# Kernel optimization log

Hardware: AMD Instinct MI355X
Metric: run time of the kernel (lower is better)

Reference implementation:

```python
import jax, jax.numpy as jnp
import numpy as np

HUGE = 1e8  # stand-in for ops.HUGE_INT

B, P, Q, PD, QD = 16, 1024, 512, 768, 768


def setup_inputs() -> dict:
    key = jax.random.key(0)
    k1, k2, k3, k4, k5 = jax.random.split(key, 5)
    p = jax.random.normal(k1, (B, P, PD), dtype=jnp.float32)
    q = jax.random.normal(k2, (B, Q, QD), dtype=jnp.float32)
    # True = padded position (masked out before softmax)
    p_masks = jax.random.randint(k3, (B, P), 0, 2).astype(bool)
    q_masks = jax.random.randint(k4, (B, Q), 0, 2).astype(bool)
    # projection weight of Linear(q_dim, p_dim, bias=False): [p_dim, q_dim]
    W = jax.random.normal(k5, (PD, QD), dtype=jnp.float32) / np.sqrt(QD)
    return {"p": p, "q": q, "p_masks": p_masks, "q_masks": q_masks, "W": W}


def reference(p, q, p_masks, q_masks, W):
    # q_proj = project(q): [B,Q,p_dim]; dropout=0.0 -> identity
    q_proj = jnp.einsum('bqd,pd->bqp', q, W)
    # affinity = p @ q_proj^T : [B,P,Q]
    affinity = jnp.einsum('bpd,bqd->bpq', p, q_proj)
    # normalize over dim 1 with padding mask broadcast over last dim
    attn_over_p = jax.nn.softmax(
        jnp.where(p_masks[:, :, None], -HUGE, affinity), axis=1)  # [B,P,Q]
    attn_over_q = jax.nn.softmax(
        jnp.where(q_masks[:, :, None], -HUGE, jnp.swapaxes(affinity, 1, 2)), axis=1)  # [B,Q,P]
    # attn(weights[B,W2,W3], cand[B,W2,C3]) -> [B,W3,C3] = weights^T @ cand
    q_to_p_attn_vec = jnp.einsum('bpq,bpd->bqd', attn_over_p, p)  # [B,Q,p_dim]
    cand = jnp.concatenate([q, q_to_p_attn_vec], axis=2)  # [B,Q,q_dim+p_dim]
    p_to_q_attn_vec = jnp.einsum('bqp,bqc->bpc', attn_over_q, cand)  # [B,P,q_dim+p_dim]
    return (p_to_q_attn_vec, q_to_p_attn_vec)
```

## Files before the change

### kernel.cpp

```cpp
#include <hip/hip_runtime.h>
#include <math.h>

constexpr int B_  = 16;
constexpr int P_  = 1024;
constexpr int Q_  = 512;
constexpr int PD_ = 768;
constexpr int QD_ = 768;
constexpr int CD_ = 1536;

#define HUGE_NEG (-1e8f)

typedef __attribute__((ext_vector_type(8))) _Float16 f16x8;
typedef __attribute__((ext_vector_type(4))) _Float16 f16x4;
typedef __attribute__((ext_vector_type(4))) float f32x4;

__device__ __forceinline__ void dma16(const void* g, void* l) {
  __builtin_amdgcn_global_load_lds((__attribute__((address_space(1))) void*)g,
                                   (__attribute__((address_space(3))) void*)l,
                                   16, 0, 0);
}

__global__ __launch_bounds__(256) void k_cvt(const float* __restrict__ src,
                                             _Float16* __restrict__ dst, int n8) {
  int i = blockIdx.x * 256 + threadIdx.x;
  if (i >= n8) return;
  float4 a = ((const float4*)src)[2 * i];
  float4 b = ((const float4*)src)[2 * i + 1];
  f16x8 o = {(_Float16)a.x, (_Float16)a.y, (_Float16)a.z, (_Float16)a.w,
             (_Float16)b.x, (_Float16)b.y, (_Float16)b.z, (_Float16)b.w};
  ((f16x8*)dst)[i] = o;
}

__global__ __launch_bounds__(256) void k_prep(const float* __restrict__ src,
                                              _Float16* __restrict__ dst16,
                                              _Float16* __restrict__ dstT,
                                              int R, int C, size_t tBatch) {
  __shared__ _Float16 T[64][72];
  int r0 = blockIdx.x * 64, c0 = blockIdx.y * 64, b = blockIdx.z;
  const float* S = src + (size_t)b * R * C;
  _Float16* D16 = dst16 + (size_t)b * R * C;
  int tid = threadIdx.x;
  int rr = tid >> 4;
  int cc = (tid & 15) * 4;
#pragma unroll
  for (int k = 0; k < 4; ++k) {
    int r = rr + k * 16;
    float4 v = *(const float4*)(S + (size_t)(r0 + r) * C + c0 + cc);
    f16x4 h = {(_Float16)v.x, (_Float16)v.y, (_Float16)v.z, (_Float16)v.w};
    *(f16x4*)(D16 + (size_t)(r0 + r) * C + c0 + cc) = h;
    T[cc + 0][r] = h[0];
    T[cc + 1][r] = h[1];
    T[cc + 2][r] = h[2];
    T[cc + 3][r] = h[3];
  }
  __syncthreads();
  int cr = tid >> 2;
  int rc = (tid & 3) * 16;
  _Float16* D = dstT + (size_t)b * tBatch + (size_t)(c0 + cr) * R + r0;
  *(f16x8*)(D + rc) = *(f16x8*)&T[cr][rc];
  *(f16x8*)(D + rc + 8) = *(f16x8*)&T[cr][rc + 8];
}

__global__ __launch_bounds__(256) void k_rowmerge(
    const float* __restrict__ rpm, const float* __restrict__ rps,
    float* __restrict__ rowmax, float* __restrict__ rowsum) {
  int idx = blockIdx.x * 256 + threadIdx.x;
  int b = idx >> 10, p = idx & 1023;
  float m = -INFINITY;
#pragma unroll
  for (int z = 0; z < 4; ++z) m = fmaxf(m, rpm[(b * 4 + z) * P_ + p]);
  float s = 0.f;
#pragma unroll
  for (int z = 0; z < 4; ++z)
    s += rps[(b * 4 + z) * P_ + p] * __expf(rpm[(b * 4 + z) * P_ + p] - m);
  rowmax[idx] = m;
  rowsum[idx] = s;
}

__global__ __launch_bounds__(256) void k_colmerge(
    const float* __restrict__ pmax_part, const float* __restrict__ psum_part,
    float* __restrict__ colmax, float* __restrict__ colsum) {
  int b = blockIdx.x;
  int q = blockIdx.y * 256 + threadIdx.x;
  float m = -INFINITY;
#pragma unroll
  for (int z = 0; z < 8; ++z) m = fmaxf(m, pmax_part[(b * 8 + z) * Q_ + q]);
  float s = 0.f;
#pragma unroll
  for (int z = 0; z < 8; ++z)
    s += psum_part[(b * 8 + z) * Q_ + q] *
         __expf(pmax_part[(b * 8 + z) * Q_ + q] - m);
  colmax[b * Q_ + q] = m;
  colsum[b * Q_ + q] = s;
}

__global__ __launch_bounds__(256) void k_w(
    const float* __restrict__ aff, const int* __restrict__ pmask,
    const int* __restrict__ qmask, const float* __restrict__ rowmax,
    const float* __restrict__ rowsum, const float* __restrict__ colmax,
    const float* __restrict__ colsum, _Float16* __restrict__ WP,
    _Float16* __restrict__ WQ) {
  __shared__ _Float16 T[64][72];
  __shared__ float rmx[64], rin[64], cmx[64], cin[64];
  int p0 = blockIdx.x * 64, q0 = blockIdx.y * 64, b = blockIdx.z;
  int tid = threadIdx.x;
  if (tid < 64) {
    rmx[tid] = rowmax[b * P_ + p0 + tid];
    rin[tid] = 1.0f / rowsum[b * P_ + p0 + tid];
  } else if (tid < 128) {
    int t = tid - 64;
    cmx[t] = colmax[b * Q_ + q0 + t];
    cin[t] = 1.0f / colsum[b * Q_ + q0 + t];
  }
  __syncthreads();
  const float* A = aff + (size_t)b * P_ * Q_;
  const int* pm = pmask + b * P_;
  int rr = tid >> 4;
  int cc = (tid & 15) * 4;
  int4 qm4 = *(const int4*)(qmask + b * Q_ + q0 + cc);
  int qm[4] = {qm4.x, qm4.y, qm4.z, qm4.w};
#pragma unroll
  for (int k = 0; k < 4; ++k) {
    int r = rr + k * 16;
    int msk = pm[p0 + r];
    float4 v = *(const float4*)(A + (size_t)(p0 + r) * Q_ + q0 + cc);
    float vv[4] = {v.x, v.y, v.z, v.w};
    f16x4 wp;
#pragma unroll
    for (int j = 0; j < 4; ++j) {
      wp[j] = (_Float16)(__expf((qm[j] ? HUGE_NEG : vv[j]) - rmx[r]) * rin[r]);
      T[cc + j][r] =
          (_Float16)(__expf((msk ? HUGE_NEG : vv[j]) - cmx[cc + j]) * cin[cc + j]);
    }
    *(f16x4*)(WP + ((size_t)b * P_ + p0 + r) * Q_ + q0 + cc) = wp;
  }
  __syncthreads();
  int cr = tid >> 2;
  int rc = (tid & 3) * 16;
  _Float16* D = WQ + ((size_t)b * Q_ + q0 + cr) * P_ + p0;
  *(f16x8*)(D + rc) = *(f16x8*)&T[cr][rc];
  *(f16x8*)(D + rc + 8) = *(f16x8*)&T[cr][rc + 8];
}

template <int NT, int LDA, int LDB>
__device__ __forceinline__ void gemm_core(const _Float16* __restrict__ Ab,
                                          const _Float16* __restrict__ Bb,
                                          _Float16* As, _Float16* Bs,
                                          f32x4 (&acc)[4][4], int w, int l) {
  constexpr int TSZ = 128 * 32;
  int rA = w * 32 + (l >> 2);
  int sA = ((l & 3) ^ ((rA >> 1) & 3)) * 8;
  int fr = l & 15;
  int fsw = (((l >> 4) ^ ((fr >> 1) & 3))) * 8;
  int wr = w >> 1, wc = w & 1;

  auto stage = [&](int buf, int t) {
    const _Float16* ga = Ab + (size_t)rA * LDA + t * 32 + sA;
    const _Float16* gb = Bb + (size_t)rA * LDB + t * 32 + sA;
    _Float16* la = As + buf * TSZ + (w * 32) * 32;
    _Float16* lb = Bs + buf * TSZ + (w * 32) * 32;
    dma16(ga, la);
    dma16(ga + 16 * LDA, la + 16 * 32);
    dma16(gb, lb);
    dma16(gb + 16 * LDB, lb + 16 * 32);
  };
  auto compute = [&](int buf) {
    const _Float16* A0 = As + buf * TSZ;
    const _Float16* B0 = Bs + buf * TSZ;
    f16x8 a[4];
#pragma unroll
    for (int m = 0; m < 4; ++m)
      a[m] = *(const f16x8*)(A0 + (wr * 64 + m * 16 + fr) * 32 + fsw);
#pragma unroll
    for (int n = 0; n < 4; ++n) {
      f16x8 bn = *(const f16x8*)(B0 + (wc * 64 + n * 16 + fr) * 32 + fsw);
#pragma unroll
      for (int m = 0; m < 4; ++m)
        acc[m][n] =
            __builtin_amdgcn_mfma_f32_16x16x32_f16(a[m], bn, acc[m][n], 0, 0, 0);
    }
  };

  stage(0, 0);
  stage(1, 1);
  int b0 = 0, b1 = 1, b2 = 2;
#pragma unroll 3
  for (int t = 0; t < NT - 2; ++t) {
    stage(b2, t + 2);
    asm volatile("s_waitcnt vmcnt(8)" ::: "memory");
    __builtin_amdgcn_s_barrier();
    __builtin_amdgcn_sched_barrier(0);
    compute(b0);
    __builtin_amdgcn_s_barrier();
    int tmp = b0; b0 = b1; b1 = b2; b2 = tmp;
  }
  asm volatile("s_waitcnt vmcnt(4)" ::: "memory");
  __builtin_amdgcn_s_barrier();
  __builtin_amdgcn_sched_barrier(0);
  compute(b0);
  __builtin_amdgcn_s_barrier();
  asm volatile("s_waitcnt vmcnt(0)" ::: "memory");
  __builtin_amdgcn_s_barrier();
  __builtin_amdgcn_sched_barrier(0);
  compute(b1);
}

#define SWZ_DECODE(GX, GY)                                          \
  int lin = blockIdx.x + (GX) * (blockIdx.y + (GY) * blockIdx.z);   \
  constexpr int NWG = (GX) * (GY) * B_;                             \
  int w8 = (lin & 7) * (NWG / 8) + (lin >> 3);                      \
  int j0 = (w8 % (GX)) * 128;                                       \
  int t_ = w8 / (GX);                                               \
  int i0 = (t_ % (GY)) * 128;                                       \
  int b = t_ / (GY);

__global__ __launch_bounds__(256) void k1_proj(const _Float16* __restrict__ q16,
                                               const _Float16* __restrict__ W16,
                                               _Float16* __restrict__ qp) {
  __shared__ alignas(16) _Float16 As[3 * 128 * 32];
  __shared__ alignas(16) _Float16 Bs[3 * 128 * 32];
  SWZ_DECODE(PD_ / 128, Q_ / 128)
  int tid = threadIdx.x, w = tid >> 6, l = tid & 63;
  f32x4 acc[4][4];
#pragma unroll
  for (int m = 0; m < 4; ++m)
#pragma unroll
    for (int n = 0; n < 4; ++n) acc[m][n] = (f32x4){0.f, 0.f, 0.f, 0.f};
  gemm_core<QD_ / 32, QD_, QD_>(q16 + (size_t)b * Q_ * QD_ + (size_t)i0 * QD_,
                                W16 + (size_t)j0 * QD_, As, Bs, acc, w, l);
  int wr = w >> 1, wc = w & 1, fr = l & 15, fq = l >> 4;
  _Float16* O = qp + (size_t)b * Q_ * PD_;
#pragma unroll
  for (int m = 0; m < 4; ++m) {
    int rl = wr * 64 + m * 16 + fq * 4;
#pragma unroll
    for (int n = 0; n < 4; ++n) {
      int cl = wc * 64 + n * 16 + fr;
#pragma unroll
      for (int r = 0; r < 4; ++r)
        O[(size_t)(i0 + rl + r) * PD_ + j0 + cl] = (_Float16)acc[m][n][r];
    }
  }
}

__global__ __launch_bounds__(256) void k2_aff(
    const _Float16* __restrict__ p16, const _Float16* __restrict__ qp,
    const int* __restrict__ pmask, const int* __restrict__ qmask,
    float* __restrict__ aff, float* __restrict__ pmax_part,
    float* __restrict__ psum_part, float* __restrict__ rpm,
    float* __restrict__ rps) {
  __shared__ alignas(16) _Float16 As[3 * 128 * 32];
  __shared__ alignas(16) _Float16 Bs[3 * 128 * 32];
  SWZ_DECODE(Q_ / 128, P_ / 128)
  int tid = threadIdx.x, w = tid >> 6, l = tid & 63;
  f32x4 acc[4][4];
#pragma unroll
  for (int m = 0; m < 4; ++m)
#pragma unroll
    for (int n = 0; n < 4; ++n) acc[m][n] = (f32x4){0.f, 0.f, 0.f, 0.f};
  gemm_core<PD_ / 32, PD_, PD_>(p16 + (size_t)b * P_ * PD_ + (size_t)i0 * PD_,
                                qp + (size_t)b * Q_ * PD_ + (size_t)j0 * PD_,
                                As, Bs, acc, w, l);
  int wr = w >> 1, wc = w & 1, fr = l & 15, fq = l >> 4;
  float* Cb = aff + (size_t)b * P_ * Q_;
#pragma unroll
  for (int m = 0; m < 4; ++m) {
    int rl = wr * 64 + m * 16 + fq * 4;
#pragma unroll
    for (int n = 0; n < 4; ++n) {
      int cl = wc * 64 + n * 16 + fr;
#pragma unroll
      for (int r = 0; r < 4; ++r)
        Cb[(size_t)(i0 + rl + r) * Q_ + j0 + cl] = acc[m][n][r];
    }
  }
  const int* pmb = pmask + b * P_ + i0;
  unsigned pmbits = 0;
#pragma unroll
  for (int m = 0; m < 4; ++m)
#pragma unroll
    for (int r = 0; r < 4; ++r)
      pmbits |= (pmb[wr * 64 + m * 16 + fq * 4 + r] ? 1u : 0u) << (m * 4 + r);
  int qmv[4];
  {
    const int* qmb = qmask + b * Q_ + j0 + wc * 64 + fr;
#pragma unroll
    for (int n = 0; n < 4; ++n) qmv[n] = qmb[n * 16];
  }
  __syncthreads();
  float* scr = (float*)As;
  float* cm_ = scr;
  float* cs_ = scr + 256;
  float* rm_ = scr + 512;
  float* rs_ = scr + 768;

#pragma unroll
  for (int n = 0; n < 4; ++n) {
    float ml = -1e30f;
#pragma unroll
    for (int m = 0; m < 4; ++m)
#pragma unroll
      for (int r = 0; r < 4; ++r) {
        float v = ((pmbits >> (m * 4 + r)) & 1) ? HUGE_NEG : acc[m][n][r];
        ml = fmaxf(ml, v);
      }
    float sl = 0.f;
#pragma unroll
    for (int m = 0; m < 4; ++m)
#pragma unroll
      for (int r = 0; r < 4; ++r) {
        float v = ((pmbits >> (m * 4 + r)) & 1) ? HUGE_NEG : acc[m][n][r];
        sl += __expf(v - ml);
      }
#pragma unroll
    for (int off = 16; off <= 32; off <<= 1) {
      float om = __shfl_xor(ml, off);
      float os = __shfl_xor(sl, off);
      float nm = fmaxf(ml, om);
      sl = sl * __expf(ml - nm) + os * __expf(om - nm);
      ml = nm;
    }
    if (fq == 0) {
      int col = wc * 64 + n * 16 + fr;
      cm_[wr * 128 + col] = ml;
      cs_[wr * 128 + col] = sl;
    }
  }
#pragma unroll
  for (int m = 0; m < 4; ++m)
#pragma unroll
    for (int r = 0; r < 4; ++r) {
      float ml = -1e30f;
#pragma unroll
      for (int n = 0; n < 4; ++n) {
        float v = qmv[n] ? HUGE_NEG : acc[m][n][r];
        ml = fmaxf(ml, v);
      }
      float sl = 0.f;
#pragma unroll
      for (int n = 0; n < 4; ++n) {
        float v = qmv[n] ? HUGE_NEG : acc[m][n][r];
        sl += __expf(v - ml);
      }
#pragma unroll
      for (int off = 1; off <= 8; off <<= 1) {
        float om = __shfl_xor(ml, off);
        float os = __shfl_xor(sl, off);
        float nm = fmaxf(ml, om);
        sl = sl * __expf(ml - nm) + os * __expf(om - nm);
        ml = nm;
      }
      if (fr == 0) {
        int row = wr * 64 + m * 16 + fq * 4 + r;
        rm_[wc * 128 + row] = ml;
        rs_[wc * 128 + row] = sl;
      }
    }
  __syncthreads();
  if (tid < 128) {
    float m0 = cm_[tid], m1 = cm_[128 + tid];
    float s0 = cs_[tid], s1 = cs_[128 + tid];
    float nm = fmaxf(m0, m1);
    float ns = s0 * __expf(m0 - nm) + s1 * __expf(m1 - nm);
    int z = i0 >> 7;
    pmax_part[(b * 8 + z) * Q_ + j0 + tid] = nm;
    psum_part[(b * 8 + z) * Q_ + j0 + tid] = ns;
  } else {
    int t = tid - 128;
    if (t < 128) {
      float m0 = rm_[t], m1 = rm_[128 + t];
      float s0 = rs_[t], s1 = rs_[128 + t];
      float nm = fmaxf(m0, m1);
      float ns = s0 * __expf(m0 - nm) + s1 * __expf(m1 - nm);
      int zj = j0 >> 7;
      rpm[(b * 4 + zj) * P_ + i0 + t] = nm;
      rps[(b * 4 + zj) * P_ + i0 + t] = ns;
    }
  }
}

__global__ __launch_bounds__(256) void k4_attn(const _Float16* __restrict__ WQ,
                                               const _Float16* __restrict__ pT,
                                               float* __restrict__ out2,
                                               _Float16* __restrict__ candT) {
  __shared__ alignas(16) _Float16 As[3 * 128 * 32];
  __shared__ alignas(16) _Float16 Bs[3 * 128 * 32];
  SWZ_DECODE(PD_ / 128, Q_ / 128)
  int tid = threadIdx.x, w = tid >> 6, l = tid & 63;
  f32x4 acc[4][4];
#pragma unroll
  for (int m = 0; m < 4; ++m)
#pragma unroll
    for (int n = 0; n < 4; ++n) acc[m][n] = (f32x4){0.f, 0.f, 0.f, 0.f};
  gemm_core<P_ / 32, P_, P_>(WQ + (size_t)b * Q_ * P_ + (size_t)i0 * P_,
                             pT + (size_t)b * PD_ * P_ + (size_t)j0 * P_, As,
                             Bs, acc, w, l);
  int wr = w >> 1, wc = w & 1, fr = l & 15, fq = l >> 4;
  float* Cb = out2 + (size_t)b * Q_ * PD_;
  _Float16* Tb = candT + (size_t)b * CD_ * Q_;
#pragma unroll
  for (int m = 0; m < 4; ++m) {
    int rl = wr * 64 + m * 16 + fq * 4;
#pragma unroll
    for (int n = 0; n < 4; ++n) {
      int cl = wc * 64 + n * 16 + fr;
      f16x4 cv;
#pragma unroll
      for (int r = 0; r < 4; ++r) {
        float v = acc[m][n][r];
        Cb[(size_t)(i0 + rl + r) * PD_ + j0 + cl] = v;
        cv[r] = (_Float16)v;
      }
      *(f16x4*)(Tb + (size_t)(QD_ + j0 + cl) * Q_ + i0 + rl) = cv;
    }
  }
}

__global__ __launch_bounds__(256) void k5_attn(const _Float16* __restrict__ WP,
                                               const _Float16* __restrict__ candT,
                                               float* __restrict__ out1) {
  __shared__ alignas(16) _Float16 As[3 * 128 * 32];
  __shared__ alignas(16) _Float16 Bs[3 * 128 * 32];
  SWZ_DECODE(CD_ / 128, P_ / 128)
  int tid = threadIdx.x, w = tid >> 6, l = tid & 63;
  f32x4 acc[4][4];
#pragma unroll
  for (int m = 0; m < 4; ++m)
#pragma unroll
    for (int n = 0; n < 4; ++n) acc[m][n] = (f32x4){0.f, 0.f, 0.f, 0.f};
  gemm_core<Q_ / 32, Q_, Q_>(WP + (size_t)b * P_ * Q_ + (size_t)i0 * Q_,
                             candT + (size_t)b * CD_ * Q_ + (size_t)j0 * Q_, As,
                             Bs, acc, w, l);
  int wr = w >> 1, wc = w & 1, fr = l & 15, fq = l >> 4;
  float* Cb = out1 + (size_t)b * P_ * CD_;
#pragma unroll
  for (int m = 0; m < 4; ++m) {
    int rl = wr * 64 + m * 16 + fq * 4;
#pragma unroll
    for (int n = 0; n < 4; ++n) {
      int cl = wc * 64 + n * 16 + fr;
#pragma unroll
      for (int r = 0; r < 4; ++r)
        Cb[(size_t)(i0 + rl + r) * CD_ + j0 + cl] = acc[m][n][r];
    }
  }
}

extern "C" void kernel_launch(void* const* d_in, const int* in_sizes, int n_in,
                              void* d_out, int out_size, void* d_ws,
                              size_t ws_size, hipStream_t stream) {
  const float* p = (const float*)d_in[0];
  const float* q = (const float*)d_in[1];
  const int* pmask = (const int*)d_in[2];
  const int* qmask = (const int*)d_in[3];
  const float* W = (const float*)d_in[4];
  float* out = (float*)d_out;

  char* ws = (char*)d_ws;
  size_t off = 0;
  auto alloc = [&](size_t bytes) {
    void* r = ws + off;
    off += (bytes + 255) & ~(size_t)255;
    return r;
  };
  _Float16* q16 = (_Float16*)alloc((size_t)B_ * Q_ * QD_ * 2);
  _Float16* p16 = (_Float16*)alloc((size_t)B_ * P_ * PD_ * 2);
  _Float16* pT = (_Float16*)alloc((size_t)B_ * PD_ * P_ * 2);
  _Float16* candT = (_Float16*)alloc((size_t)B_ * CD_ * Q_ * 2);
  _Float16* W16 = (_Float16*)alloc((size_t)PD_ * QD_ * 2);
  _Float16* qp16 = (_Float16*)alloc((size_t)B_ * Q_ * PD_ * 2);
  float* aff = (float*)alloc((size_t)B_ * P_ * Q_ * 4);
  _Float16* WP = (_Float16*)alloc((size_t)B_ * P_ * Q_ * 2);
  _Float16* WQ = (_Float16*)alloc((size_t)B_ * Q_ * P_ * 2);
  float* rowmax = (float*)alloc((size_t)B_ * P_ * 4);
  float* rowsum = (float*)alloc((size_t)B_ * P_ * 4);
  float* colmax = (float*)alloc((size_t)B_ * Q_ * 4);
  float* colsum = (float*)alloc((size_t)B_ * Q_ * 4);
  float* pmax_part = (float*)alloc((size_t)B_ * 8 * Q_ * 4);
  float* psum_part = (float*)alloc((size_t)B_ * 8 * Q_ * 4);
  float* rpm = (float*)alloc((size_t)B_ * 4 * P_ * 4);
  float* rps = (float*)alloc((size_t)B_ * 4 * P_ * 4);

  float* out1 = out;
  float* out2 = out + (size_t)B_ * P_ * CD_;

  k_cvt<<<PD_ * QD_ / 8 / 256, 256, 0, stream>>>(W, W16, PD_ * QD_ / 8);
  k_prep<<<dim3(Q_ / 64, QD_ / 64, B_), 256, 0, stream>>>(
      q, q16, candT, Q_, QD_, (size_t)CD_ * Q_);
  k_prep<<<dim3(P_ / 64, PD_ / 64, B_), 256, 0, stream>>>(
      p, p16, pT, P_, PD_, (size_t)PD_ * P_);
  k1_proj<<<dim3(PD_ / 128, Q_ / 128, B_), 256, 0, stream>>>(q16, W16, qp16);
  k2_aff<<<dim3(Q_ / 128, P_ / 128, B_), 256, 0, stream>>>(
      p16, qp16, pmask, qmask, aff, pmax_part, psum_part, rpm, rps);
  k_rowmerge<<<B_ * P_ / 256, 256, 0, stream>>>(rpm, rps, rowmax, rowsum);
  k_colmerge<<<dim3(B_, Q_ / 256), 256, 0, stream>>>(pmax_part, psum_part,
                                                     colmax, colsum);
  k_w<<<dim3(P_ / 64, Q_ / 64, B_), 256, 0, stream>>>(
      aff, pmask, qmask, rowmax, rowsum, colmax, colsum, WP, WQ);
  k4_attn<<<dim3(PD_ / 128, Q_ / 128, B_), 256, 0, stream>>>(WQ, pT, out2,
                                                             candT);
  k5_attn<<<dim3(CD_ / 128, P_ / 128, B_), 256, 0, stream>>>(WP, candT, out1);
}
```

Before: 168.2 us.

## Enlarge GEMM tiles to 256x128 with 8 waves and fold softmax merges into k_w

```diff
diff --git a/kernel.cpp b/kernel.cpp
--- a/kernel.cpp
+++ b/kernel.cpp
@@ -61,56 +61,40 @@
   *(f16x8*)(D + rc + 8) = *(f16x8*)&T[cr][rc + 8];
 }
 
-__global__ __launch_bounds__(256) void k_rowmerge(
-    const float* __restrict__ rpm, const float* __restrict__ rps,
-    float* __restrict__ rowmax, float* __restrict__ rowsum) {
-  int idx = blockIdx.x * 256 + threadIdx.x;
-  int b = idx >> 10, p = idx & 1023;
-  float m = -INFINITY;
-#pragma unroll
-  for (int z = 0; z < 4; ++z) m = fmaxf(m, rpm[(b * 4 + z) * P_ + p]);
-  float s = 0.f;
-#pragma unroll
-  for (int z = 0; z < 4; ++z)
-    s += rps[(b * 4 + z) * P_ + p] * __expf(rpm[(b * 4 + z) * P_ + p] - m);
-  rowmax[idx] = m;
-  rowsum[idx] = s;
-}
-
-__global__ __launch_bounds__(256) void k_colmerge(
-    const float* __restrict__ pmax_part, const float* __restrict__ psum_part,
-    float* __restrict__ colmax, float* __restrict__ colsum) {
-  int b = blockIdx.x;
-  int q = blockIdx.y * 256 + threadIdx.x;
-  float m = -INFINITY;
-#pragma unroll
-  for (int z = 0; z < 8; ++z) m = fmaxf(m, pmax_part[(b * 8 + z) * Q_ + q]);
-  float s = 0.f;
-#pragma unroll
-  for (int z = 0; z < 8; ++z)
-    s += psum_part[(b * 8 + z) * Q_ + q] *
-         __expf(pmax_part[(b * 8 + z) * Q_ + q] - m);
-  colmax[b * Q_ + q] = m;
-  colsum[b * Q_ + q] = s;
-}
-
 __global__ __launch_bounds__(256) void k_w(
     const float* __restrict__ aff, const int* __restrict__ pmask,
-    const int* __restrict__ qmask, const float* __restrict__ rowmax,
-    const float* __restrict__ rowsum, const float* __restrict__ colmax,
-    const float* __restrict__ colsum, _Float16* __restrict__ WP,
+    const int* __restrict__ qmask, const float* __restrict__ rpm,
+    const float* __restrict__ rps, const float* __restrict__ pmax_part,
+    const float* __restrict__ psum_part, _Float16* __restrict__ WP,
     _Float16* __restrict__ WQ) {
   __shared__ _Float16 T[64][72];
   __shared__ float rmx[64], rin[64], cmx[64], cin[64];
   int p0 = blockIdx.x * 64, q0 = blockIdx.y * 64, b = blockIdx.z;
   int tid = threadIdx.x;
   if (tid < 64) {
-    rmx[tid] = rowmax[b * P_ + p0 + tid];
-    rin[tid] = 1.0f / rowsum[b * P_ + p0 + tid];
+    int pp = p0 + tid;
+    float m = -INFINITY;
+#pragma unroll
+    for (int z = 0; z < 4; ++z) m = fmaxf(m, rpm[(b * 4 + z) * P_ + pp]);
+    float s = 0.f;
+#pragma unroll
+    for (int z = 0; z < 4; ++z)
+      s += rps[(b * 4 + z) * P_ + pp] * __expf(rpm[(b * 4 + z) * P_ + pp] - m);
+    rmx[tid] = m;
+    rin[tid] = 1.0f / s;
   } else if (tid < 128) {
     int t = tid - 64;
-    cmx[t] = colmax[b * Q_ + q0 + t];
-    cin[t] = 1.0f / colsum[b * Q_ + q0 + t];
+    int qq = q0 + t;
+    float m = -INFINITY;
+#pragma unroll
+    for (int z = 0; z < 4; ++z) m = fmaxf(m, pmax_part[(b * 4 + z) * Q_ + qq]);
+    float s = 0.f;
+#pragma unroll
+    for (int z = 0; z < 4; ++z)
+      s += psum_part[(b * 4 + z) * Q_ + qq] *
+           __expf(pmax_part[(b * 4 + z) * Q_ + qq] - m);
+    cmx[t] = m;
+    cin[t] = 1.0f / s;
   }
   __syncthreads();
   const float* A = aff + (size_t)b * P_ * Q_;
@@ -147,26 +131,26 @@
                                           const _Float16* __restrict__ Bb,
                                           _Float16* As, _Float16* Bs,
                                           f32x4 (&acc)[4][4], int w, int l) {
-  constexpr int TSZ = 128 * 32;
+  constexpr int ASZ = 256 * 32, BSZ = 128 * 32;
   int rA = w * 32 + (l >> 2);
-  int sA = ((l & 3) ^ ((rA >> 1) & 3)) * 8;
+  int rB = w * 16 + (l >> 2);
+  int sk = ((l & 3) ^ ((l >> 3) & 3)) * 8;
   int fr = l & 15;
   int fsw = (((l >> 4) ^ ((fr >> 1) & 3))) * 8;
   int wr = w >> 1, wc = w & 1;
 
   auto stage = [&](int buf, int t) {
-    const _Float16* ga = Ab + (size_t)rA * LDA + t * 32 + sA;
-    const _Float16* gb = Bb + (size_t)rA * LDB + t * 32 + sA;
-    _Float16* la = As + buf * TSZ + (w * 32) * 32;
-    _Float16* lb = Bs + buf * TSZ + (w * 32) * 32;
+    const _Float16* ga = Ab + (size_t)rA * LDA + t * 32 + sk;
+    const _Float16* gb = Bb + (size_t)rB * LDB + t * 32 + sk;
+    _Float16* la = As + buf * ASZ + (w * 32) * 32;
+    _Float16* lb = Bs + buf * BSZ + (w * 16) * 32;
     dma16(ga, la);
     dma16(ga + 16 * LDA, la + 16 * 32);
     dma16(gb, lb);
-    dma16(gb + 16 * LDB, lb + 16 * 32);
   };
   auto compute = [&](int buf) {
-    const _Float16* A0 = As + buf * TSZ;
-    const _Float16* B0 = Bs + buf * TSZ;
+    const _Float16* A0 = As + buf * ASZ;
+    const _Float16* B0 = Bs + buf * BSZ;
     f16x8 a[4];
 #pragma unroll
     for (int m = 0; m < 4; ++m)
@@ -187,14 +171,14 @@
 #pragma unroll 3
   for (int t = 0; t < NT - 2; ++t) {
     stage(b2, t + 2);
-    asm volatile("s_waitcnt vmcnt(8)" ::: "memory");
+    asm volatile("s_waitcnt vmcnt(6)" ::: "memory");
     __builtin_amdgcn_s_barrier();
     __builtin_amdgcn_sched_barrier(0);
     compute(b0);
     __builtin_amdgcn_s_barrier();
     int tmp = b0; b0 = b1; b1 = b2; b2 = tmp;
   }
-  asm volatile("s_waitcnt vmcnt(4)" ::: "memory");
+  asm volatile("s_waitcnt vmcnt(3)" ::: "memory");
   __builtin_amdgcn_s_barrier();
   __builtin_amdgcn_sched_barrier(0);
   compute(b0);
@@ -211,15 +195,15 @@
   int w8 = (lin & 7) * (NWG / 8) + (lin >> 3);                      \
   int j0 = (w8 % (GX)) * 128;                                       \
   int t_ = w8 / (GX);                                               \
-  int i0 = (t_ % (GY)) * 128;                                       \
+  int i0 = (t_ % (GY)) * 256;                                       \
   int b = t_ / (GY);
 
-__global__ __launch_bounds__(256) void k1_proj(const _Float16* __restrict__ q16,
-                                               const _Float16* __restrict__ W16,
-                                               _Float16* __restrict__ qp) {
-  __shared__ alignas(16) _Float16 As[3 * 128 * 32];
+__global__ __launch_bounds__(512, 4) void k1_proj(
+    const _Float16* __restrict__ q16, const _Float16* __restrict__ W16,
+    _Float16* __restrict__ qp) {
+  __shared__ alignas(16) _Float16 As[3 * 256 * 32];
   __shared__ alignas(16) _Float16 Bs[3 * 128 * 32];
-  SWZ_DECODE(PD_ / 128, Q_ / 128)
+  SWZ_DECODE(PD_ / 128, Q_ / 256)
   int tid = threadIdx.x, w = tid >> 6, l = tid & 63;
   f32x4 acc[4][4];
 #pragma unroll
@@ -243,15 +227,15 @@
   }
 }
 
-__global__ __launch_bounds__(256) void k2_aff(
+__global__ __launch_bounds__(512, 4) void k2_aff(
     const _Float16* __restrict__ p16, const _Float16* __restrict__ qp,
     const int* __restrict__ pmask, const int* __restrict__ qmask,
     float* __restrict__ aff, float* __restrict__ pmax_part,
     float* __restrict__ psum_part, float* __restrict__ rpm,
     float* __restrict__ rps) {
-  __shared__ alignas(16) _Float16 As[3 * 128 * 32];
+  __shared__ alignas(16) _Float16 As[3 * 256 * 32];
   __shared__ alignas(16) _Float16 Bs[3 * 128 * 32];
-  SWZ_DECODE(Q_ / 128, P_ / 128)
+  SWZ_DECODE(Q_ / 128, P_ / 256)
   int tid = threadIdx.x, w = tid >> 6, l = tid & 63;
   f32x4 acc[4][4];
 #pragma unroll
@@ -290,9 +274,9 @@
   __syncthreads();
   float* scr = (float*)As;
   float* cm_ = scr;
-  float* cs_ = scr + 256;
-  float* rm_ = scr + 512;
-  float* rs_ = scr + 768;
+  float* cs_ = scr + 512;
+  float* rm_ = scr + 1024;
+  float* rs_ = scr + 1536;
 
 #pragma unroll
   for (int n = 0; n < 4; ++n) {
@@ -352,40 +336,39 @@
       }
       if (fr == 0) {
         int row = wr * 64 + m * 16 + fq * 4 + r;
-        rm_[wc * 128 + row] = ml;
-        rs_[wc * 128 + row] = sl;
+        rm_[wc * 256 + row] = ml;
+        rs_[wc * 256 + row] = sl;
       }
     }
   __syncthreads();
   if (tid < 128) {
-    float m0 = cm_[tid], m1 = cm_[128 + tid];
-    float s0 = cs_[tid], s1 = cs_[128 + tid];
+    float nm = fmaxf(fmaxf(cm_[tid], cm_[128 + tid]),
+                     fmaxf(cm_[256 + tid], cm_[384 + tid]));
+    float ns = cs_[tid] * __expf(cm_[tid] - nm) +
+               cs_[128 + tid] * __expf(cm_[128 + tid] - nm) +
+               cs_[256 + tid] * __expf(cm_[256 + tid] - nm) +
+               cs_[384 + tid] * __expf(cm_[384 + tid] - nm);
+    int z = i0 >> 8;
+    pmax_part[(b * 4 + z) * Q_ + j0 + tid] = nm;
+    psum_part[(b * 4 + z) * Q_ + j0 + tid] = ns;
+  } else if (tid >= 256) {
+    int t = tid - 256;
+    float m0 = rm_[t], m1 = rm_[256 + t];
+    float s0 = rs_[t], s1 = rs_[256 + t];
     float nm = fmaxf(m0, m1);
     float ns = s0 * __expf(m0 - nm) + s1 * __expf(m1 - nm);
-    int z = i0 >> 7;
-    pmax_part[(b * 8 + z) * Q_ + j0 + tid] = nm;
-    psum_part[(b * 8 + z) * Q_ + j0 + tid] = ns;
-  } else {
-    int t = tid - 128;
-    if (t < 128) {
-      float m0 = rm_[t], m1 = rm_[128 + t];
-      float s0 = rs_[t], s1 = rs_[128 + t];
-      float nm = fmaxf(m0, m1);
-      float ns = s0 * __expf(m0 - nm) + s1 * __expf(m1 - nm);
-      int zj = j0 >> 7;
-      rpm[(b * 4 + zj) * P_ + i0 + t] = nm;
-      rps[(b * 4 + zj) * P_ + i0 + t] = ns;
-    }
-  }
-}
-
-__global__ __launch_bounds__(256) void k4_attn(const _Float16* __restrict__ WQ,
-                                               const _Float16* __restrict__ pT,
-                                               float* __restrict__ out2,
-                                               _Float16* __restrict__ candT) {
-  __shared__ alignas(16) _Float16 As[3 * 128 * 32];
+    int zj = j0 >> 7;
+    rpm[(b * 4 + zj) * P_ + i0 + t] = nm;
+    rps[(b * 4 + zj) * P_ + i0 + t] = ns;
+  }
+}
+
+__global__ __launch_bounds__(512, 4) void k4_attn(
+    const _Float16* __restrict__ WQ, const _Float16* __restrict__ pT,
+    float* __restrict__ out2, _Float16* __restrict__ candT) {
+  __shared__ alignas(16) _Float16 As[3 * 256 * 32];
   __shared__ alignas(16) _Float16 Bs[3 * 128 * 32];
-  SWZ_DECODE(PD_ / 128, Q_ / 128)
+  SWZ_DECODE(PD_ / 128, Q_ / 256)
   int tid = threadIdx.x, w = tid >> 6, l = tid & 63;
   f32x4 acc[4][4];
 #pragma unroll
@@ -416,12 +399,12 @@
   }
 }
 
-__global__ __launch_bounds__(256) void k5_attn(const _Float16* __restrict__ WP,
-                                               const _Float16* __restrict__ candT,
-                                               float* __restrict__ out1) {
-  __shared__ alignas(16) _Float16 As[3 * 128 * 32];
+__global__ __launch_bounds__(512, 4) void k5_attn(
+    const _Float16* __restrict__ WP, const _Float16* __restrict__ candT,
+    float* __restrict__ out1) {
+  __shared__ alignas(16) _Float16 As[3 * 256 * 32];
   __shared__ alignas(16) _Float16 Bs[3 * 128 * 32];
-  SWZ_DECODE(CD_ / 128, P_ / 128)
+  SWZ_DECODE(CD_ / 128, P_ / 256)
   int tid = threadIdx.x, w = tid >> 6, l = tid & 63;
   f32x4 acc[4][4];
 #pragma unroll
@@ -472,12 +455,8 @@
   float* aff = (float*)alloc((size_t)B_ * P_ * Q_ * 4);
   _Float16* WP = (_Float16*)alloc((size_t)B_ * P_ * Q_ * 2);
   _Float16* WQ = (_Float16*)alloc((size_t)B_ * Q_ * P_ * 2);
-  float* rowmax = (float*)alloc((size_t)B_ * P_ * 4);
-  float* rowsum = (float*)alloc((size_t)B_ * P_ * 4);
-  float* colmax = (float*)alloc((size_t)B_ * Q_ * 4);
-  float* colsum = (float*)alloc((size_t)B_ * Q_ * 4);
-  float* pmax_part = (float*)alloc((size_t)B_ * 8 * Q_ * 4);
-  float* psum_part = (float*)alloc((size_t)B_ * 8 * Q_ * 4);
+  float* pmax_part = (float*)alloc((size_t)B_ * 4 * Q_ * 4);
+  float* psum_part = (float*)alloc((size_t)B_ * 4 * Q_ * 4);
   float* rpm = (float*)alloc((size_t)B_ * 4 * P_ * 4);
   float* rps = (float*)alloc((size_t)B_ * 4 * P_ * 4);
 
@@ -489,15 +468,12 @@
       q, q16, candT, Q_, QD_, (size_t)CD_ * Q_);
   k_prep<<<dim3(P_ / 64, PD_ / 64, B_), 256, 0, stream>>>(
       p, p16, pT, P_, PD_, (size_t)PD_ * P_);
-  k1_proj<<<dim3(PD_ / 128, Q_ / 128, B_), 256, 0, stream>>>(q16, W16, qp16);
-  k2_aff<<<dim3(Q_ / 128, P_ / 128, B_), 256, 0, stream>>>(
+  k1_proj<<<dim3(PD_ / 128, Q_ / 256, B_), 512, 0, stream>>>(q16, W16, qp16);
+  k2_aff<<<dim3(Q_ / 128, P_ / 256, B_), 512, 0, stream>>>(
       p16, qp16, pmask, qmask, aff, pmax_part, psum_part, rpm, rps);
-  k_rowmerge<<<B_ * P_ / 256, 256, 0, stream>>>(rpm, rps, rowmax, rowsum);
-  k_colmerge<<<dim3(B_, Q_ / 256), 256, 0, stream>>>(pmax_part, psum_part,
-                                                     colmax, colsum);
   k_w<<<dim3(P_ / 64, Q_ / 64, B_), 256, 0, stream>>>(
-      aff, pmask, qmask, rowmax, rowsum, colmax, colsum, WP, WQ);
-  k4_attn<<<dim3(PD_ / 128, Q_ / 128, B_), 256, 0, stream>>>(WQ, pT, out2,
+      aff, pmask, qmask, rpm, rps, pmax_part, psum_part, WP, WQ);
+  k4_attn<<<dim3(PD_ / 128, Q_ / 256, B_), 512, 0, stream>>>(WQ, pT, out2,
                                                              candT);
-  k5_attn<<<dim3(CD_ / 128, P_ / 128, B_), 256, 0, stream>>>(WP, candT, out1);
-}
+  k5_attn<<<dim3(CD_ / 128, P_ / 256, B_), 512, 0, stream>>>(WP, candT, out1);
+}
```

After: 168.0 us. Within noise of the previous version (-0.1%).
